# Performance work log

Hardware: AMD Instinct MI355X
Metric: run time of the kernel (lower is better)

## Reference

```python
import jax, jax.numpy as jnp
import numpy as np
from functools import partial

V, H, B, T, L = 32000, 1024, 64, 64, 4
EOS = 2


def setup_inputs() -> dict:
    key = jax.random.key(0)
    ks = jax.random.split(key, 10)
    s = 1.0 / np.sqrt(H)
    return {
        "max_len": T,
        "tgt": jax.random.randint(ks[0], (B, T), 0, V),
        "h0": jax.random.normal(ks[1], (L, B, H), jnp.float32),
        "c0": jax.random.normal(ks[2], (L, B, H), jnp.float32),
        "embedding": jax.random.normal(ks[3], (V, H), jnp.float32) * s,
        "W_ih": jax.random.normal(ks[4], (L, 4 * H, H), jnp.float32) * s,
        "W_hh": jax.random.normal(ks[5], (L, 4 * H, H), jnp.float32) * s,
        "b_ih": jax.random.normal(ks[6], (L, 4 * H), jnp.float32) * s,
        "b_hh": jax.random.normal(ks[7], (L, 4 * H), jnp.float32) * s,
        "W_cls": jax.random.normal(ks[8], (V, H), jnp.float32) * s,
        "b_cls": jax.random.normal(ks[9], (V,), jnp.float32) * s,
    }


def _lstm_cell(x, h, c, Wi, Wh, bi, bh):
    # gates: [B, 4H] in torch order (i, f, g, o)
    g = x @ Wi.T + bi + h @ Wh.T + bh
    i, f, gg, o = jnp.split(g, 4, axis=-1)
    c2 = jax.nn.sigmoid(f) * c + jax.nn.sigmoid(i) * jnp.tanh(gg)
    h2 = jax.nn.sigmoid(o) * jnp.tanh(c2)
    return h2, c2


def reference(max_len, tgt, h0, c0, embedding, W_ih, W_hh, b_ih, b_hh, W_cls, b_cls):
    # step i>0 uses embedding of tgt[:, i-1].
    batch = tgt.shape[0]
    x0 = jnp.broadcast_to(embedding[EOS], (batch, embedding.shape[1]))
    tf_in = embedding[tgt[:, : max_len - 1]]              # [B, T-1, H]
    inputs = jnp.concatenate([x0[:, None, :], tf_in], axis=1)  # [B, T, H]
    inputs = jnp.swapaxes(inputs, 0, 1)                   # [T, B, H]

    def step(carry, x):
        h, c = carry  # each [L, B, H]
        hs, cs = [], []
        inp = x
        for l in range(L):  # 4 stacked LSTM cells, h of cell l feeds cell l+1
            hn, cn = _lstm_cell(inp, h[l], c[l], W_ih[l], W_hh[l], b_ih[l], b_hh[l])
            hs.append(hn)
            cs.append(cn)
            inp = hn
        h = jnp.stack(hs)
        c = jnp.stack(cs)
        logp = jax.nn.log_softmax(h[L - 1] @ W_cls.T + b_cls, axis=-1)  # [B, V]
        return (h, c), logp

    (h, c), out = jax.lax.scan(step, (h0, c0), inputs)
    return out, h, c  # out: [T, B, V]
```

## Files before the change

kernel.cpp:

```cpp
#include <hip/hip_runtime.h>

using u16 = unsigned short;
using u32 = unsigned int;

typedef __bf16 bf16x8 __attribute__((ext_vector_type(8)));
typedef float  f32x4  __attribute__((ext_vector_type(4)));
typedef u16    u16x8  __attribute__((ext_vector_type(8)));

static constexpr int kV = 32000, kH = 1024, kB = 64, kT = 64, kL = 4, kEOS = 2;

struct Flag { int v; int pad[15]; };

__device__ __forceinline__ u16 f2bf(float f) {
  u32 u = __float_as_uint(f);
  u = (u + 0x7fffu + ((u >> 16) & 1u)) >> 16;
  return (u16)u;
}
__device__ __forceinline__ float sigf(float x)   { return 1.0f / (1.0f + __expf(-x)); }
__device__ __forceinline__ float tanhf_(float x) { return 1.0f - 2.0f / (__expf(2.0f * x) + 1.0f); }

typedef const __attribute__((address_space(1))) u32* gas_ptr;
typedef __attribute__((address_space(3))) u32*       las_ptr;
__device__ __forceinline__ void async16(const u16* g, u16* l) {
  __builtin_amdgcn_global_load_lds((gas_ptr)g, (las_ptr)l, 16, 0, 0);
}

__device__ __forceinline__ void spin_ge(const int* p, int tgt) {
  while (__hip_atomic_load(p, __ATOMIC_RELAXED, __HIP_MEMORY_SCOPE_AGENT) < tgt)
    __builtin_amdgcn_s_sleep(2);
}

__device__ __forceinline__ size_t packed_off(int b, int k) {
  return (size_t)(((b >> 4) * 32 + (k >> 5)) * 512 + (((k >> 3) & 3) * 16 + (b & 15)) * 8 + (k & 7));
}


__global__ void pack_lstm(const float* __restrict__ Wih, const float* __restrict__ Whh,
                          u16* __restrict__ wpack) {
  const int cid  = blockIdx.x * 256 + threadIdx.x;
  const int lane = cid & 63;
  const int cf   = (cid >> 6) & 3;
  const int kk   = (cid >> 8) & 31;
  const int mt   = (cid >> 13) & 1;
  const int blk  = cid >> 14;
  const int lay = blk >> 6, cb = blk & 63;
  const int wr = cf * 1024 + cb * 16 + (lane & 15);
  const int kb = kk * 32 + (lane >> 4) * 8;
  const float* src = (mt ? Whh : Wih) + ((size_t)lay * 4096 + wr) * 1024 + kb;
  const float4* s4 = (const float4*)src;
  float4 v0 = s4[0], v1 = s4[1];
  u16x8 r;
  r[0]=f2bf(v0.x); r[1]=f2bf(v0.y); r[2]=f2bf(v0.z); r[3]=f2bf(v0.w);
  r[4]=f2bf(v1.x); r[5]=f2bf(v1.y); r[6]=f2bf(v1.z); r[7]=f2bf(v1.w);
  *(u16x8*)(wpack + (size_t)cid * 8) = r;
}

__global__ void pack_cls(const float* __restrict__ W, u16* __restrict__ o) {
  const size_t cid = (size_t)blockIdx.x * 256 + threadIdx.x;
  const float4* s4 = (const float4*)(W + cid * 8);
  float4 v0 = s4[0], v1 = s4[1];
  u16x8 r;
  r[0]=f2bf(v0.x); r[1]=f2bf(v0.y); r[2]=f2bf(v0.z); r[3]=f2bf(v0.w);
  r[4]=f2bf(v1.x); r[5]=f2bf(v1.y); r[6]=f2bf(v1.z); r[7]=f2bf(v1.w);
  *(u16x8*)(o + cid * 8) = r;
}

__global__ void pack_x(const float* __restrict__ emb, const int* __restrict__ tgt,
                       u16* __restrict__ X) {
  const int cid = blockIdx.x * 256 + threadIdx.x;
  const int kc = cid & 127, b = (cid >> 7) & 63, t = cid >> 13;
  const int tok = (t == 0) ? kEOS : tgt[b * 64 + t - 1];
  const float4* s4 = (const float4*)(emb + (size_t)tok * 1024 + kc * 8);
  float4 v0 = s4[0], v1 = s4[1];
  u16x8 r;
  r[0]=f2bf(v0.x); r[1]=f2bf(v0.y); r[2]=f2bf(v0.z); r[3]=f2bf(v0.w);
  r[4]=f2bf(v1.x); r[5]=f2bf(v1.y); r[6]=f2bf(v1.z); r[7]=f2bf(v1.w);
  *(u16x8*)(X + (size_t)t * 65536 + packed_off(b, kc * 8)) = r;
}

__global__ void pack_init(const float* __restrict__ h0, const float* __restrict__ bih,
                          const float* __restrict__ bhh, u16* __restrict__ hball,
                          float* __restrict__ bsum) {
  const int cid = blockIdx.x * 256 + threadIdx.x;
  if (cid < 32768) {
    const int kc = cid & 127, row = cid >> 7;
    const int lay = row >> 6, b = row & 63;
    const float4* s4 = (const float4*)(h0 + (size_t)cid * 8);
    float4 v0 = s4[0], v1 = s4[1];
    u16x8 r;
    r[0]=f2bf(v0.x); r[1]=f2bf(v0.y); r[2]=f2bf(v0.z); r[3]=f2bf(v0.w);
    r[4]=f2bf(v1.x); r[5]=f2bf(v1.y); r[6]=f2bf(v1.z); r[7]=f2bf(v1.w);
    *(u16x8*)(hball + (size_t)lay * 65 * 65536 + packed_off(b, kc * 8)) = r;
  } else {
    const int i = cid - 32768;
    bsum[i] = bih[i] + bhh[i];
  }
}

__global__ void __launch_bounds__(1024, 4)
lstm_coop(const u16* __restrict__ wpack, const u16* __restrict__ xall,
          u16* __restrict__ hball, const float* __restrict__ bsum,
          const float* __restrict__ c0, float* __restrict__ outh, float* __restrict__ outc,
          Flag* flags) {
  __shared__ u16 stg[2][32][512];
  __shared__ float Gc[4][64][66];

  const int tid = threadIdx.x, lane = tid & 63, wave = tid >> 6;
  const int l15 = lane & 15, l4 = lane >> 4;
  const int cmat = wave >> 3, cwc = (wave >> 1) & 3, ckh = wave & 1;
  const int blk = blockIdx.x, lay = blk >> 6, cb = blk & 63, u0 = cb << 4;
  const int ub = tid >> 4, uu = tid & 15;

  float creg = c0[((size_t)lay * 64 + ub) * 1024 + u0 + uu];
  float bsv[4];
  #pragma unroll
  for (int g = 0; g < 4; ++g) bsv[g] = bsum[lay * 4096 + g * 1024 + u0 + uu];

  const size_t wbase = (size_t)blk * 131072;
  bf16x8 breg[16];
  #pragma unroll
  for (int j = 0; j < 16; ++j)
    breg[j] = *(const bf16x8*)(wpack + wbase
        + (size_t)(((cmat * 32 + 2 * j + ckh) * 4) + cwc) * 512 + lane * 8);

  const int j0 = wave * 2, j1 = wave * 2 + 1;
  const int m2a = j0 >> 4, mta = (j0 >> 2) & 3, ksla = j0 & 3;
  const int m2b = j1 >> 4, mtb = (j1 >> 2) & 3, kslb = j1 & 3;

  u16* hlay = hball + (size_t)lay * 65 * 65536;
  const u16* hprev = (lay == 0) ? xall : (hball + (size_t)(lay - 1) * 65 * 65536);

  #pragma unroll 1
  for (int t = 0; t < kT; ++t) {
    if (t > 0 && tid < 64)                 spin_ge(&flags[lay * 64 + tid].v, t);
    if (lay > 0 && tid >= 64 && tid < 128) spin_ge(&flags[(lay - 1) * 64 + (tid - 64)].v, t + 1);
    __syncthreads();

    const u16* xsrc = (lay == 0) ? (xall + (size_t)t * 65536)
                                 : (hprev + (size_t)(t + 1) * 65536);
    const u16* hsrc = hlay + (size_t)t * 65536;

    const u16* ga = (m2a ? hsrc : xsrc) + (size_t)((mta * 32 + ksla) * 512) + lane * 8;
    const u16* gb = (m2b ? hsrc : xsrc) + (size_t)((mtb * 32 + kslb) * 512) + lane * 8;
    u16* da = &stg[0][m2a * 16 + mta * 4 + ksla][0];
    u16* db = &stg[0][m2b * 16 + mtb * 4 + kslb][0];

    auto STAGE = [&](int c) {
      async16(ga + (size_t)c * 2048, da + (c & 1) * 16384);
      async16(gb + (size_t)c * 2048, db + (c & 1) * 16384);
    };

    f32x4 acc[4] = {};
    STAGE(0);
    #pragma unroll
    for (int c = 0; c < 8; ++c) {
      asm volatile("s_waitcnt vmcnt(0)" ::: "memory");
      __builtin_amdgcn_s_barrier();
      asm volatile("" ::: "memory");
      if (c < 7) STAGE(c + 1);
      const u16* As = &stg[c & 1][cmat * 16][0];
      #pragma unroll
      for (int s = 0; s < 2; ++s) {
        const int ksl = 2 * s + ckh;
        bf16x8 a[4];
        #pragma unroll
        for (int m = 0; m < 4; ++m)
          a[m] = *(const bf16x8*)(As + (m * 4 + ksl) * 512 + lane * 8);
        #pragma unroll
        for (int m = 0; m < 4; ++m)
          acc[m] = __builtin_amdgcn_mfma_f32_16x16x32_bf16(a[m], breg[2 * c + s], acc[m], 0, 0, 0);
      }
    }

    {
      const int q = cmat * 2 + ckh;
      #pragma unroll
      for (int m = 0; m < 4; ++m)
        #pragma unroll
        for (int r = 0; r < 4; ++r)
          Gc[q][m * 16 + l4 * 4 + r][cwc * 16 + l15] = acc[m][r];
    }
    __syncthreads();

    float sg[4];
    #pragma unroll
    for (int g = 0; g < 4; ++g) {
      const int col = g * 16 + uu;
      sg[g] = Gc[0][ub][col] + Gc[1][ub][col] + Gc[2][ub][col] + Gc[3][ub][col] + bsv[g];
    }
    const float c2 = sigf(sg[1]) * creg + sigf(sg[0]) * tanhf_(sg[2]);
    const float h2 = sigf(sg[3]) * tanhf_(c2);
    creg = c2;
    const u16 hv = f2bf(h2);
    if (t == kT - 1) {
      outh[((size_t)lay * 64 + ub) * 1024 + u0 + uu] = h2;
      outc[((size_t)lay * 64 + ub) * 1024 + u0 + uu] = c2;
    }
    const u32 other = __shfl_xor((u32)hv, 1);
    if ((tid & 1) == 0) {
      const u32 hpair = (u32)hv | (other << 16);
      u32* hdst = (u32*)(hlay + (size_t)(t + 1) * 65536 + packed_off(ub, u0 + uu));
      __hip_atomic_store(hdst, hpair, __ATOMIC_RELAXED, __HIP_MEMORY_SCOPE_AGENT);
    }
    __syncthreads();
    if (tid == 0)
      __hip_atomic_store(&flags[lay * 64 + cb].v, t + 1, __ATOMIC_RELAXED, __HIP_MEMORY_SCOPE_AGENT);
  }
}

#define CLS_EPILOGUE()                                                                     \
  {                                                                                        \
    float* sR = (float*)&sA[0][0];                                                         \
    _Pragma("unroll")                                                                      \
    for (int mi = 0; mi < 4; ++mi) {                                                       \
      _Pragma("unroll")                                                                    \
      for (int r = 0; r < 4; ++r) {                                                        \
        float v[4];                                                                        \
        _Pragma("unroll")                                                                  \
        for (int ci = 0; ci < 4; ++ci) v[ci] = acc[mi][ci][r] + bc[ci];                     \
        float mx = fmaxf(fmaxf(v[0], v[1]), fmaxf(v[2], v[3]));                            \
        mx = fmaxf(mx, __shfl_xor(mx, 1)); mx = fmaxf(mx, __shfl_xor(mx, 2));              \
        mx = fmaxf(mx, __shfl_xor(mx, 4)); mx = fmaxf(mx, __shfl_xor(mx, 8));              \
        float ss = __expf(v[0]-mx) + __expf(v[1]-mx) + __expf(v[2]-mx) + __expf(v[3]-mx);  \
        ss += __shfl_xor(ss, 1); ss += __shfl_xor(ss, 2);                                  \
        ss += __shfl_xor(ss, 4); ss += __shfl_xor(ss, 8);                                  \
        const int lr = wm * 64 + mi * 16 + l4 * 4 + r;                                     \
        if (wc == 0 && l15 == 0) { sR[lr * 2] = mx; sR[lr * 2 + 1] = ss; }                 \
        __syncthreads();                                                                   \
        if (wc == 1 && l15 == 0) {                                                         \
          const float m0 = sR[lr * 2], s0 = sR[lr * 2 + 1];                                \
          const float M = fmaxf(m0, mx);                                                   \
          const float S = s0 * __expf(m0 - M) + ss * __expf(mx - M);                       \
          const int grow = bm * 128 + lr;                                                  \
          pmax[(size_t)grow * 256 + bn] = M;                                               \
          psum[(size_t)grow * 256 + bn] = S;                                               \
        }                                                                                  \
        __syncthreads();                                                                   \
      }                                                                                    \
    }                                                                                      \
  }

__global__ void __launch_bounds__(256)
cls_gemm(const u16* __restrict__ A, const u16* __restrict__ Bw,
         const float* __restrict__ bcls, float* __restrict__ out,
         float* __restrict__ pmax, float* __restrict__ psum) {
  __shared__ u16 sA[2][4096], sB[2][4096];
  const int tid = threadIdx.x, lane = tid & 63, wave = tid >> 6;
  const int wm = wave >> 1, wc = wave & 1;
  const int l15 = lane & 15, l4 = lane >> 4;
  const int bn = blockIdx.x, bm = blockIdx.y;
  const u16* Ab = A  + (size_t)bm * 131072;
  const u16* Bb = Bw + (size_t)bn * 131072;

  auto STAGE = [&](int kk) {
    u16* dA = sA[kk & 1]; u16* dB = sB[kk & 1];
    #pragma unroll
    for (int q = 0; q < 4; ++q) {
      const int u = wave * 4 + q;
      if (u < 8) {
        const u16* g = Ab + (size_t)(u >> 2) * 65536 + (size_t)(((u & 3) * 32 + kk) * 512) + lane * 8;
        async16(g, dA + u * 512);
      } else {
        const int v = u & 7;
        const u16* g = Bb + (size_t)((v & 1) * 64 + lane) * 1024 + kk * 32 + (v >> 1) * 8;
        async16(g, dB + v * 512);
      }
    }
  };

  f32x4 acc[4][4] = {};
  STAGE(0);
  for (int kk = 0; kk < 32; ++kk) {
    if (kk < 31) { STAGE(kk + 1); asm volatile("s_waitcnt vmcnt(4)" ::: "memory"); }
    else         asm volatile("s_waitcnt vmcnt(0)" ::: "memory");
    __builtin_amdgcn_s_barrier();
    asm volatile("" ::: "memory");
    const u16* aS = sA[kk & 1]; const u16* bS = sB[kk & 1];
    bf16x8 av[4], bv[4];
    #pragma unroll
    for (int mi = 0; mi < 4; ++mi) av[mi] = *(const bf16x8*)(aS + (wm * 4 + mi) * 512 + lane * 8);
    #pragma unroll
    for (int ci = 0; ci < 4; ++ci) bv[ci] = *(const bf16x8*)(bS + l4 * 1024 + (wc * 64 + ci * 16 + l15) * 8);
    #pragma unroll
    for (int mi = 0; mi < 4; ++mi)
      #pragma unroll
      for (int ci = 0; ci < 4; ++ci)
        acc[mi][ci] = __builtin_amdgcn_mfma_f32_16x16x32_bf16(av[mi], bv[ci], acc[mi][ci], 0, 0, 0);
    asm volatile("" ::: "memory");
    __builtin_amdgcn_s_barrier();
  }
  float bc[4];
  #pragma unroll
  for (int ci = 0; ci < 4; ++ci) bc[ci] = bcls[bn * 128 + wc * 64 + ci * 16 + l15];
  #pragma unroll
  for (int ci = 0; ci < 4; ++ci) {
    const int col = bn * 128 + wc * 64 + ci * 16 + l15;
    #pragma unroll
    for (int mi = 0; mi < 4; ++mi)
      #pragma unroll
      for (int r = 0; r < 4; ++r) {
        const int row = bm * 128 + wm * 64 + mi * 16 + l4 * 4 + r;
        out[(size_t)row * 32000 + col] = acc[mi][ci][r] + bc[ci];
      }
  }
  __syncthreads();
  CLS_EPILOGUE()
}

__global__ void __launch_bounds__(256)
cls_gemm_f32(const u16* __restrict__ A, const float* __restrict__ Bw,
             const float* __restrict__ bcls, float* __restrict__ out,
             float* __restrict__ pmax, float* __restrict__ psum) {
  __shared__ u16 sA[2][4096], sB[2][4096];
  const int tid = threadIdx.x, lane = tid & 63, wave = tid >> 6;
  const int wm = wave >> 1, wc = wave & 1;
  const int l15 = lane & 15, l4 = lane >> 4;
  const int bn = blockIdx.x, bm = blockIdx.y;
  const u16*  Ab = A  + (size_t)bm * 131072;
  const float* Bb = Bw + (size_t)bn * 131072;

  auto LOADB = [&](int kk, u16x8* rb) {
    #pragma unroll
    for (int q = 0; q < 2; ++q) {
      const int p = tid + q * 256, row = p & 127, khi = p >> 7;
      const float4* s4 = (const float4*)(Bb + (size_t)row * 1024 + kk * 32 + khi * 8);
      float4 v0 = s4[0], v1 = s4[1];
      u16x8 r;
      r[0]=f2bf(v0.x); r[1]=f2bf(v0.y); r[2]=f2bf(v0.z); r[3]=f2bf(v0.w);
      r[4]=f2bf(v1.x); r[5]=f2bf(v1.y); r[6]=f2bf(v1.z); r[7]=f2bf(v1.w);
      rb[q] = r;
    }
  };
  auto WRITEB = [&](int kk, const u16x8* rb) {
    u16* dB = sB[kk & 1];
    #pragma unroll
    for (int q = 0; q < 2; ++q) *(u16x8*)(dB + (tid + q * 256) * 8) = rb[q];
  };
  auto STAGE_A = [&](int kk) {
    u16* dA = sA[kk & 1];
    #pragma unroll
    for (int q = 0; q < 2; ++q) {
      const int v = wave * 2 + q;
      const u16* g = Ab + (size_t)(v >> 2) * 65536 + (size_t)(((v & 3) * 32 + kk) * 512) + lane * 8;
      async16(g, dA + v * 512);
    }
  };

  f32x4 acc[4][4] = {};
  {
    u16x8 rb[2];
    LOADB(0, rb); STAGE_A(0); WRITEB(0, rb);
  }
  for (int kk = 0; kk < 32; ++kk) {
    if (kk < 31) {
      u16x8 rb[2];
      LOADB(kk + 1, rb);
      STAGE_A(kk + 1);
      WRITEB(kk + 1, rb);
    } else {
      asm volatile("s_waitcnt vmcnt(0)" ::: "memory");
    }
    __builtin_amdgcn_s_barrier();
    asm volatile("" ::: "memory");
    const u16* aS = sA[kk & 1]; const u16* bS = sB[kk & 1];
    bf16x8 av[4], bv[4];
    #pragma unroll
    for (int mi = 0; mi < 4; ++mi) av[mi] = *(const bf16x8*)(aS + (wm * 4 + mi) * 512 + lane * 8);
    #pragma unroll
    for (int ci = 0; ci < 4; ++ci) bv[ci] = *(const bf16x8*)(bS + l4 * 1024 + (wc * 64 + ci * 16 + l15) * 8);
    #pragma unroll
    for (int mi = 0; mi < 4; ++mi)
      #pragma unroll
      for (int ci = 0; ci < 4; ++ci)
        acc[mi][ci] = __builtin_amdgcn_mfma_f32_16x16x32_bf16(av[mi], bv[ci], acc[mi][ci], 0, 0, 0);
    asm volatile("" ::: "memory");
    __builtin_amdgcn_s_barrier();
  }
  float bc[4];
  #pragma unroll
  for (int ci = 0; ci < 4; ++ci) bc[ci] = bcls[bn * 128 + wc * 64 + ci * 16 + l15];
  #pragma unroll
  for (int ci = 0; ci < 4; ++ci) {
    const int col = bn * 128 + wc * 64 + ci * 16 + l15;
    #pragma unroll
    for (int mi = 0; mi < 4; ++mi)
      #pragma unroll
      for (int r = 0; r < 4; ++r) {
        const int row = bm * 128 + wm * 64 + mi * 16 + l4 * 4 + r;
        out[(size_t)row * 32000 + col] = acc[mi][ci][r] + bc[ci];
      }
  }
  __syncthreads();
  CLS_EPILOGUE()
}

__global__ void __launch_bounds__(256)
lsm_red(const float* __restrict__ pmax, const float* __restrict__ psum,
        float* __restrict__ logz) {
  __shared__ float rm[256], rs[256];
  const int r = blockIdx.x, b = threadIdx.x;
  float m = -3.0e38f, s = 0.0f;
  if (b < 250) { m = pmax[(size_t)r * 256 + b]; s = psum[(size_t)r * 256 + b]; }
  rm[b] = m; rs[b] = s; __syncthreads();
  for (int st = 128; st > 0; st >>= 1) {
    if (b < st) {
      const float m2 = rm[b + st], s2 = rs[b + st];
      const float M = fmaxf(rm[b], m2);
      rs[b] = rs[b] * __expf(rm[b] - M) + s2 * __expf(m2 - M);
      rm[b] = M;
    }
    __syncthreads();
  }
  if (b == 0) logz[r] = rm[0] + logf(rs[0]);
}

__global__ void __launch_bounds__(256)
sub_k(float* __restrict__ out, const float* __restrict__ logz) {
  const int r = blockIdx.x;
  const float z = logz[r];
  float4* p = (float4*)(out + (size_t)r * 32000);
  for (int v = threadIdx.x; v < 8000; v += 256) {
    float4 x = p[v];
    x.x -= z; x.y -= z; x.z -= z; x.w -= z;
    p[v] = x;
  }
}

extern "C" void kernel_launch(void* const* d_in, const int* in_sizes, int n_in,
                              void* d_out, int out_size, void* d_ws, size_t ws_size,
                              hipStream_t stream) {
  (void)in_sizes; (void)n_in; (void)out_size;
  const int*   tgt  = (const int*)d_in[1];
  const float* h0   = (const float*)d_in[2];
  const float* c0   = (const float*)d_in[3];
  const float* emb  = (const float*)d_in[4];
  const float* Wih  = (const float*)d_in[5];
  const float* Whh  = (const float*)d_in[6];
  const float* bih  = (const float*)d_in[7];
  const float* bhh  = (const float*)d_in[8];
  const float* Wcls = (const float*)d_in[9];
  const float* bcls = (const float*)d_in[10];

  float* out  = (float*)d_out;
  float* outh = out + (size_t)kT * kB * kV;
  float* outc = outh + (size_t)kL * kB * kH;

  const size_t SZ_WPACK = 67108864;
  const size_t SZ_WCLS  = 65536000;
  const size_t SZ_X     = 8388608;
  const size_t SZ_HBALL = 34078720;
  const size_t SZ_BSUM  = 65536;
  const size_t SZ_FLAGS = 16384;
  const size_t SZ_PM    = 4194304;
  const size_t FULL_REQ = SZ_WPACK + SZ_WCLS + SZ_X + SZ_HBALL + SZ_BSUM + SZ_FLAGS + 2 * SZ_PM + 16384;
  const bool full = (ws_size >= FULL_REQ);

  char* ws = (char*)d_ws;
  size_t off = 0;
  u16* wpack = (u16*)(ws + off); off += SZ_WPACK;
  u16* wclsb = nullptr;
  if (full) { wclsb = (u16*)(ws + off); off += SZ_WCLS; }
  u16*   X     = (u16*)(ws + off); off += SZ_X;
  u16*   hball = (u16*)(ws + off); off += SZ_HBALL;
  float* bsum  = (float*)(ws + off); off += SZ_BSUM;
  Flag*  flags = (Flag*)(ws + off);  off += SZ_FLAGS;
  float* pmax  = (float*)(ws + off); off += SZ_PM;
  float* psum  = (float*)(ws + off); off += SZ_PM;
  float* logz  = (float*)(ws + off); off += 16384;

  pack_lstm<<<16384, 256, 0, stream>>>(Wih, Whh, wpack);
  if (full) pack_cls<<<16000, 256, 0, stream>>>(Wcls, wclsb);
  pack_x   <<<2048,  256, 0, stream>>>(emb, tgt, X);
  pack_init<<<192,   256, 0, stream>>>(h0, bih, bhh, hball, bsum);
  hipMemsetAsync(flags, 0, SZ_FLAGS, stream);

  void* args[] = { (void*)&wpack, (void*)&X, (void*)&hball, (void*)&bsum,
                   (void*)&c0, (void*)&outh, (void*)&outc, (void*)&flags };
  hipLaunchCooperativeKernel((const void*)lstm_coop, dim3(256), dim3(1024), args, 0, stream);

  const u16* h3a = hball + (size_t)3 * 65 * 65536 + 65536;
  if (full) cls_gemm    <<<dim3(250, 32), 256, 0, stream>>>(h3a, wclsb, bcls, out, pmax, psum);
  else      cls_gemm_f32<<<dim3(250, 32), 256, 0, stream>>>(h3a, Wcls,  bcls, out, pmax, psum);
  lsm_red<<<4096, 256, 0, stream>>>(pmax, psum, logz);
  sub_k  <<<4096, 256, 0, stream>>>(out, logz);
}
```

Before: 1.414 ms.

## Triple-buffer LSTM staging, remap block-to-layer mapping, and halve gate reduction buffer

Staging of x/h tiles moves from double to triple buffering, keeping two async loads in flight (vmcnt(2)) so global latency overlaps more of the MFMA work. The block-to-(layer, column-block) mapping is permuted so blocks of different layers interleave across block IDs, likely spreading each layer's blocks across XCDs/CUs. The k-split reduction buffer shrinks from 4 to 2 slices, using an extra barrier and a read-modify-write in LDS to free shared memory for the third stage buffer. The extra __syncthreads adds a little per-step latency on the serial recurrence path.

New measurement: 1.365 ms. -3.5%, faster.

```diff
diff --git a/kernel.cpp b/kernel.cpp
--- a/kernel.cpp
+++ b/kernel.cpp
@@ -102,13 +102,16 @@
           u16* __restrict__ hball, const float* __restrict__ bsum,
           const float* __restrict__ c0, float* __restrict__ outh, float* __restrict__ outc,
           Flag* flags) {
-  __shared__ u16 stg[2][32][512];
-  __shared__ float Gc[4][64][66];
+  __shared__ u16 stg[3][32][512];
+  __shared__ float Gc[2][64][66];
 
   const int tid = threadIdx.x, lane = tid & 63, wave = tid >> 6;
   const int l15 = lane & 15, l4 = lane >> 4;
   const int cmat = wave >> 3, cwc = (wave >> 1) & 3, ckh = wave & 1;
-  const int blk = blockIdx.x, lay = blk >> 6, cb = blk & 63, u0 = cb << 4;
+  const int blk = blockIdx.x;
+  const int lay = (blk >> 1) & 3;
+  const int cb  = ((blk >> 3) << 1) | (blk & 1);
+  const int u0 = cb << 4;
   const int ub = tid >> 4, uu = tid & 15;
 
   float creg = c0[((size_t)lay * 64 + ub) * 1024 + u0 + uu];
@@ -116,7 +119,7 @@
   #pragma unroll
   for (int g = 0; g < 4; ++g) bsv[g] = bsum[lay * 4096 + g * 1024 + u0 + uu];
 
-  const size_t wbase = (size_t)blk * 131072;
+  const size_t wbase = (size_t)(lay * 64 + cb) * 131072;
   bf16x8 breg[16];
   #pragma unroll
   for (int j = 0; j < 16; ++j)
@@ -142,23 +145,22 @@
 
     const u16* ga = (m2a ? hsrc : xsrc) + (size_t)((mta * 32 + ksla) * 512) + lane * 8;
     const u16* gb = (m2b ? hsrc : xsrc) + (size_t)((mtb * 32 + kslb) * 512) + lane * 8;
-    u16* da = &stg[0][m2a * 16 + mta * 4 + ksla][0];
-    u16* db = &stg[0][m2b * 16 + mtb * 4 + kslb][0];
 
     auto STAGE = [&](int c) {
-      async16(ga + (size_t)c * 2048, da + (c & 1) * 16384);
-      async16(gb + (size_t)c * 2048, db + (c & 1) * 16384);
+      async16(ga + (size_t)c * 2048, &stg[c % 3][m2a * 16 + mta * 4 + ksla][0]);
+      async16(gb + (size_t)c * 2048, &stg[c % 3][m2b * 16 + mtb * 4 + kslb][0]);
     };
 
     f32x4 acc[4] = {};
-    STAGE(0);
+    STAGE(0); STAGE(1);
     #pragma unroll
     for (int c = 0; c < 8; ++c) {
-      asm volatile("s_waitcnt vmcnt(0)" ::: "memory");
+      if (c < 7) asm volatile("s_waitcnt vmcnt(2)" ::: "memory");
+      else       asm volatile("s_waitcnt vmcnt(0)" ::: "memory");
       __builtin_amdgcn_s_barrier();
       asm volatile("" ::: "memory");
-      if (c < 7) STAGE(c + 1);
-      const u16* As = &stg[c & 1][cmat * 16][0];
+      if (c < 6) STAGE(c + 2);
+      const u16* As = &stg[c % 3][cmat * 16][0];
       #pragma unroll
       for (int s = 0; s < 2; ++s) {
         const int ksl = 2 * s + ckh;
@@ -172,13 +174,20 @@
       }
     }
 
-    {
-      const int q = cmat * 2 + ckh;
+    if (ckh == 0) {
       #pragma unroll
       for (int m = 0; m < 4; ++m)
         #pragma unroll
         for (int r = 0; r < 4; ++r)
-          Gc[q][m * 16 + l4 * 4 + r][cwc * 16 + l15] = acc[m][r];
+          Gc[cmat][m * 16 + l4 * 4 + r][cwc * 16 + l15] = acc[m][r];
+    }
+    __syncthreads();
+    if (ckh == 1) {
+      #pragma unroll
+      for (int m = 0; m < 4; ++m)
+        #pragma unroll
+        for (int r = 0; r < 4; ++r)
+          Gc[cmat][m * 16 + l4 * 4 + r][cwc * 16 + l15] += acc[m][r];
     }
     __syncthreads();
 
@@ -186,7 +195,7 @@
     #pragma unroll
     for (int g = 0; g < 4; ++g) {
       const int col = g * 16 + uu;
-      sg[g] = Gc[0][ub][col] + Gc[1][ub][col] + Gc[2][ub][col] + Gc[3][ub][col] + bsv[g];
+      sg[g] = Gc[0][ub][col] + Gc[1][ub][col] + bsv[g];
     }
     const float c2 = sigf(sg[1]) * creg + sigf(sg[0]) * tanhf_(sg[2]);
     const float h2 = sigf(sg[3]) * tanhf_(c2);
```
